# Kernel optimization log

Hardware: AMD Instinct MI355X
Metric: run time of the kernel (lower is better)

The kernel has to match this reference:

```python
import jax, jax.numpy as jnp
import numpy as np

N_CHANNELS = 8
SECTION = 32768
F_IN = 64
F_OUT = 64
UNITS = 512


def setup_inputs() -> dict:
    key = jax.random.key(0)
    ks = jax.random.split(key, 10)
    scale = lambda fan_in: 1.0 / np.sqrt(fan_in)
    return {
        "x": jax.random.normal(ks[0], (N_CHANNELS * SECTION, F_IN), jnp.float32),
        "w0": jax.random.normal(ks[1], (N_CHANNELS, UNITS, F_IN), jnp.float32) * scale(F_IN),
        "w1": jax.random.normal(ks[2], (N_CHANNELS, UNITS, UNITS), jnp.float32) * scale(UNITS),
        "w2": jax.random.normal(ks[3], (N_CHANNELS, UNITS, UNITS), jnp.float32) * scale(UNITS),
        "w3": jax.random.normal(ks[4], (N_CHANNELS, F_OUT, UNITS), jnp.float32) * scale(UNITS),
        "b0": jax.random.normal(ks[5], (N_CHANNELS, UNITS), jnp.float32) * 0.01,
        "b1": jax.random.normal(ks[6], (N_CHANNELS, UNITS), jnp.float32) * 0.01,
        "b2": jax.random.normal(ks[7], (N_CHANNELS, UNITS), jnp.float32) * 0.01,
        "b3": jax.random.normal(ks[8], (N_CHANNELS, F_OUT), jnp.float32) * 0.01,
        "section_size": SECTION,
    }


def reference(x, w0, w1, w2, w3, b0, b1, b2, b3, section_size):
    # Equal sections of size `section_size` per channel: reshape to [C, S, F]
    # and run the per-channel MLP as batched (grouped) GEMMs.
    C = w0.shape[0]
    xs = x.reshape(C, section_size, -1)  # [C, S, F_in]
    for w, b in ((w0, b0), (w1, b1), (w2, b2)):
        xs = jax.nn.relu(jnp.einsum('csi,coi->cso', xs, w) + b[:, None, :])
    ys = jnp.einsum('csi,coi->cso', xs, w3) + b3[:, None, :]  # [C, S, F_out]
    return ys.reshape(C * section_size, -1)
```

## Files before the change

### kernel.cpp

```cpp
#include <hip/hip_runtime.h>
#include <hip/hip_bf16.h>

#define CH 8
#define SEC 32768
#define FIN 64
#define FOUT 64
#define UN 512
#define BM 64

typedef __bf16 bf16;
typedef bf16 bf16x8 __attribute__((ext_vector_type(8)));
typedef bf16 bf16x4 __attribute__((ext_vector_type(4)));
typedef float f32x4 __attribute__((ext_vector_type(4)));

__device__ __forceinline__ bf16x8 cvt8(const float* __restrict__ src) {
  f32x4 u0 = *(const f32x4*)src;
  f32x4 u1 = *(const f32x4*)(src + 4);
  bf16x8 v;
  v[0] = (bf16)u0[0]; v[1] = (bf16)u0[1]; v[2] = (bf16)u0[2]; v[3] = (bf16)u0[3];
  v[4] = (bf16)u1[0]; v[5] = (bf16)u1[1]; v[6] = (bf16)u1[2]; v[7] = (bf16)u1[3];
  return v;
}

__device__ __forceinline__ void store_cvt8(void* dst, const float* __restrict__ src) {
  *(bf16x8*)dst = cvt8(src);
}

template<int K, bool WSPATH>
__device__ __forceinline__ void run_main_layer(
    const bf16* __restrict__ wb,
    const float* __restrict__ wf,
    const float* __restrict__ bias, char* __restrict__ act,
    int w, int l, int l15, int l4)
{
  constexpr int NKS = K / 32;
  const int col0 = w * 64;
  const char* abase = act + l * 16;

  f32x4 acc[4][4];
#pragma unroll
  for (int mt = 0; mt < 4; ++mt)
#pragma unroll
    for (int nt = 0; nt < 4; ++nt)
      acc[mt][nt] = f32x4{0.f, 0.f, 0.f, 0.f};

  if constexpr (WSPATH) {
    const bf16* bp = wb + ((size_t)(w * 4) * NKS * 64 + l) * 8;
    bf16x8 B0[4], B1[4];
#pragma unroll
    for (int i = 0; i < 4; ++i)
      B0[i] = *(const bf16x8*)(bp + (size_t)(i * NKS) * 512);

#pragma unroll
    for (int j = 0; j < NKS; j += 2) {
      if (j + 1 < NKS) {
#pragma unroll
        for (int i = 0; i < 4; ++i)
          B1[i] = *(const bf16x8*)(bp + (size_t)(i * NKS + j + 1) * 512);
      }
      {
        bf16x8 a[4];
#pragma unroll
        for (int mt = 0; mt < 4; ++mt)
          a[mt] = *(const bf16x8*)(abase + (mt * NKS + j) * 1024);
        __builtin_amdgcn_s_setprio(1);
#pragma unroll
        for (int mt = 0; mt < 4; ++mt)
#pragma unroll
          for (int nt = 0; nt < 4; ++nt)
            acc[mt][nt] = __builtin_amdgcn_mfma_f32_16x16x32_bf16(B0[nt], a[mt], acc[mt][nt], 0, 0, 0);
        __builtin_amdgcn_s_setprio(0);
      }
      if (j + 2 < NKS) {
#pragma unroll
        for (int i = 0; i < 4; ++i)
          B0[i] = *(const bf16x8*)(bp + (size_t)(i * NKS + j + 2) * 512);
      }
      if (j + 1 < NKS) {
        bf16x8 a[4];
#pragma unroll
        for (int mt = 0; mt < 4; ++mt)
          a[mt] = *(const bf16x8*)(abase + (mt * NKS + j + 1) * 1024);
        __builtin_amdgcn_s_setprio(1);
#pragma unroll
        for (int mt = 0; mt < 4; ++mt)
#pragma unroll
          for (int nt = 0; nt < 4; ++nt)
            acc[mt][nt] = __builtin_amdgcn_mfma_f32_16x16x32_bf16(B1[nt], a[mt], acc[mt][nt], 0, 0, 0);
        __builtin_amdgcn_s_setprio(0);
      }
    }
  } else {
    const float* bpf[4];
#pragma unroll
    for (int nt = 0; nt < 4; ++nt)
      bpf[nt] = wf + (size_t)(col0 + nt * 16 + l15) * K + l4 * 8;
#pragma unroll
    for (int j = 0; j < NKS; ++j) {
      bf16x8 a[4], b[4];
#pragma unroll
      for (int nt = 0; nt < 4; ++nt) b[nt] = cvt8(bpf[nt] + j * 32);
#pragma unroll
      for (int mt = 0; mt < 4; ++mt)
        a[mt] = *(const bf16x8*)(abase + (mt * NKS + j) * 1024);
#pragma unroll
      for (int mt = 0; mt < 4; ++mt)
#pragma unroll
        for (int nt = 0; nt < 4; ++nt)
          acc[mt][nt] = __builtin_amdgcn_mfma_f32_16x16x32_bf16(b[nt], a[mt], acc[mt][nt], 0, 0, 0);
    }
  }

  __syncthreads();

#pragma unroll
  for (int nt = 0; nt < 4; ++nt) {
    const f32x4 bv = *(const f32x4*)(bias + col0 + nt * 16 + l4 * 4);
    const int slot = l15 + ((nt & 1) * 2 + (l4 >> 1)) * 16;
    const int ksp  = w * 2 + (nt >> 1);
    const int boff = slot * 16 + (l4 & 1) * 8;
#pragma unroll
    for (int mt = 0; mt < 4; ++mt) {
      bf16x4 pk;
#pragma unroll
      for (int r = 0; r < 4; ++r) {
        const float v = acc[mt][nt][r] + bv[r];
        pk[r] = (bf16)(v > 0.f ? v : 0.f);
      }
      *(bf16x4*)(act + (mt * 16 + ksp) * 1024 + boff) = pk;
    }
  }
  __syncthreads();
}

template<bool WSPATH>
__device__ __forceinline__ void run_final_layer(
    const bf16* __restrict__ wb, const float* __restrict__ wf,
    const float* __restrict__ bias, const char* __restrict__ act,
    float* __restrict__ gout,
    int w, int l, int l15, int l4)
{
  constexpr int NKS = 16;
  const int mt = w >> 1;
  const int nb = (w & 1) * 2;
  const char* abase = act + mt * 16384 + l * 16;

  f32x4 acc[2];
  acc[0] = f32x4{0.f, 0.f, 0.f, 0.f};
  acc[1] = f32x4{0.f, 0.f, 0.f, 0.f};

  if constexpr (WSPATH) {
    const bf16* bp0 = wb + ((size_t)(nb + 0) * 16 * 64 + l) * 8;
    const bf16* bp1 = wb + ((size_t)(nb + 1) * 16 * 64 + l) * 8;
    bf16x8 B0[2], B1[2];
    B0[0] = *(const bf16x8*)(bp0);
    B0[1] = *(const bf16x8*)(bp1);
#pragma unroll
    for (int j = 0; j < NKS; j += 2) {
      {
        B1[0] = *(const bf16x8*)(bp0 + (size_t)(j + 1) * 512);
        B1[1] = *(const bf16x8*)(bp1 + (size_t)(j + 1) * 512);
        const bf16x8 a = *(const bf16x8*)(abase + j * 1024);
        acc[0] = __builtin_amdgcn_mfma_f32_16x16x32_bf16(B0[0], a, acc[0], 0, 0, 0);
        acc[1] = __builtin_amdgcn_mfma_f32_16x16x32_bf16(B0[1], a, acc[1], 0, 0, 0);
      }
      {
        if (j + 2 < NKS) {
          B0[0] = *(const bf16x8*)(bp0 + (size_t)(j + 2) * 512);
          B0[1] = *(const bf16x8*)(bp1 + (size_t)(j + 2) * 512);
        }
        const bf16x8 a = *(const bf16x8*)(abase + (j + 1) * 1024);
        acc[0] = __builtin_amdgcn_mfma_f32_16x16x32_bf16(B1[0], a, acc[0], 0, 0, 0);
        acc[1] = __builtin_amdgcn_mfma_f32_16x16x32_bf16(B1[1], a, acc[1], 0, 0, 0);
      }
    }
  } else {
    const float* bpf0 = wf + (size_t)((nb + 0) * 16 + l15) * UN + l4 * 8;
    const float* bpf1 = wf + (size_t)((nb + 1) * 16 + l15) * UN + l4 * 8;
#pragma unroll
    for (int j = 0; j < NKS; ++j) {
      const bf16x8 b0 = cvt8(bpf0 + j * 32);
      const bf16x8 b1 = cvt8(bpf1 + j * 32);
      const bf16x8 a = *(const bf16x8*)(abase + j * 1024);
      acc[0] = __builtin_amdgcn_mfma_f32_16x16x32_bf16(b0, a, acc[0], 0, 0, 0);
      acc[1] = __builtin_amdgcn_mfma_f32_16x16x32_bf16(b1, a, acc[1], 0, 0, 0);
    }
  }

#pragma unroll
  for (int i = 0; i < 2; ++i) {
    const f32x4 bv = *(const f32x4*)(bias + (nb + i) * 16 + l4 * 4);
    f32x4 o;
#pragma unroll
    for (int r = 0; r < 4; ++r) o[r] = acc[i][r] + bv[r];
    *(f32x4*)(gout + (size_t)(mt * 16 + l15) * FOUT + (nb + i) * 16 + l4 * 4) = o;
  }
}

template<bool WSPATH>
__global__ __launch_bounds__(512, 2) void mlp_fused(
    const float* __restrict__ x,
    const float* __restrict__ w0f, const float* __restrict__ w1f,
    const float* __restrict__ w2f, const float* __restrict__ w3f,
    const float* __restrict__ b0, const float* __restrict__ b1,
    const float* __restrict__ b2, const float* __restrict__ b3,
    const bf16* __restrict__ wbase,
    float* __restrict__ out)
{
  extern __shared__ char smem[];
  char* act = smem;

  const int tid = threadIdx.x;
  const int w = tid >> 6, l = tid & 63;
  const int l15 = l & 15, l4 = l >> 4;

  const int wg = (blockIdx.x & 7) * 512 + (blockIdx.x >> 3);
  const int ch = wg >> 9;
  const int row0 = (wg & 511) * BM;

  const bf16* w0b = wbase + (size_t)ch * UN * FIN;
  const bf16* w1b = wbase + CH * UN * FIN + (size_t)ch * UN * UN;
  const bf16* w2b = wbase + CH * UN * FIN + CH * UN * UN + (size_t)ch * UN * UN;
  const bf16* w3b = wbase + CH * UN * FIN + 2 * CH * UN * UN + (size_t)ch * FOUT * UN;
  const float* w0c = w0f + (size_t)ch * UN * FIN;
  const float* w1c = w1f + (size_t)ch * UN * UN;
  const float* w2c = w2f + (size_t)ch * UN * UN;
  const float* w3c = w3f + (size_t)ch * FOUT * UN;
  const float* b0c = b0 + ch * UN;
  const float* b1c = b1 + ch * UN;
  const float* b2c = b2 + ch * UN;
  const float* b3c = b3 + ch * FOUT;

  {
    const float* xs = x + (size_t)(ch * SEC + row0) * FIN;
    store_cvt8(act + w * 1024 + l * 16,
               xs + ((w >> 1) * 16 + l15) * FIN + (w & 1) * 32 + l4 * 8);
  }
  __syncthreads();

  run_main_layer<64,  WSPATH>(w0b, w0c, b0c, act, w, l, l15, l4);
  run_main_layer<512, WSPATH>(w1b, w1c, b1c, act, w, l, l15, l4);
  run_main_layer<512, WSPATH>(w2b, w2c, b2c, act, w, l, l15, l4);
  run_final_layer<WSPATH>(w3b, w3c, b3c, act,
                          out + (size_t)(ch * SEC + row0) * FOUT,
                          w, l, l15, l4);
}

template<int K, int N>
__device__ __forceinline__ void cvt_one(const float* __restrict__ src,
                                        bf16* __restrict__ dst, int t)
{
  constexpr int NKS = K / 32;
  constexpr int perCh = N * K / 8;
  const int ch = t / perCh;
  const int r = t - ch * perCh;
  const int l = r & 63;
  const int p = r >> 6;
  const int ks = p & (NKS - 1);
  const int f = p / NKS;
  const float* s = src + (size_t)ch * N * K + (size_t)(f * 16 + (l & 15)) * K
                 + ks * 32 + (l >> 4) * 8;
  store_cvt8(dst + (size_t)t * 8, s);
}

__global__ void cvt_weights(const float* __restrict__ w0, const float* __restrict__ w1,
                            const float* __restrict__ w2, const float* __restrict__ w3,
                            bf16* __restrict__ o)
{
  constexpr int T0 = CH * UN * FIN / 8;
  constexpr int T1 = CH * UN * UN / 8;
  constexpr int total = 2 * T0 + 2 * T1;
  for (int t = blockIdx.x * blockDim.x + threadIdx.x; t < total;
       t += gridDim.x * blockDim.x) {
    if (t < T0)                cvt_one<FIN, UN>(w0, o, t);
    else if (t < T0 + T1)      cvt_one<UN, UN>(w1, o + CH * UN * FIN, t - T0);
    else if (t < T0 + 2 * T1)  cvt_one<UN, UN>(w2, o + CH * UN * FIN + CH * UN * UN, t - T0 - T1);
    else                       cvt_one<UN, FOUT>(w3, o + CH * UN * FIN + 2 * CH * UN * UN, t - T0 - 2 * T1);
  }
}

extern "C" void kernel_launch(void* const* d_in, const int* in_sizes, int n_in,
                              void* d_out, int out_size, void* d_ws, size_t ws_size,
                              hipStream_t stream)
{
  const float* x  = (const float*)d_in[0];
  const float* w0 = (const float*)d_in[1];
  const float* w1 = (const float*)d_in[2];
  const float* w2 = (const float*)d_in[3];
  const float* w3 = (const float*)d_in[4];
  const float* b0 = (const float*)d_in[5];
  const float* b1 = (const float*)d_in[6];
  const float* b2 = (const float*)d_in[7];
  const float* b3 = (const float*)d_in[8];
  float* out = (float*)d_out;

  const int grid = CH * (SEC / BM);
  const size_t wbytes = (size_t)(2 * CH * UN * FIN + 2 * CH * UN * UN) * 2;

  if (ws_size >= wbytes) {
    bf16* wb = (bf16*)d_ws;
    hipLaunchKernelGGL(cvt_weights, dim3(2304), dim3(256), 0, stream, w0, w1, w2, w3, wb);
    hipFuncSetAttribute(reinterpret_cast<const void*>(mlp_fused<true>),
                        hipFuncAttributeMaxDynamicSharedMemorySize, 65536);
    hipLaunchKernelGGL(mlp_fused<true>, dim3(grid), dim3(512), 65536, stream,
                       x, w0, w1, w2, w3, b0, b1, b2, b3, wb, out);
  } else {
    hipFuncSetAttribute(reinterpret_cast<const void*>(mlp_fused<false>),
                        hipFuncAttributeMaxDynamicSharedMemorySize, 65536);
    hipLaunchKernelGGL(mlp_fused<false>, dim3(grid), dim3(512), 65536, stream,
                       x, w0, w1, w2, w3, b0, b1, b2, b3, (const bf16*)nullptr, out);
  }
}
```

Before: 302.8 us.

## Double row tile to 128 with 16-wave 2x8 warp grid per block

Raises the rows per block from 64 to 128 and launches 1024-thread blocks, with waves arranged as 2 row groups by 8 column groups. Each weight fragment loaded from global memory now feeds twice as many rows, which cuts weight traffic per row. The final layer is remapped so each wave handles one 16-column group across two row tiles. In exchange the block needs 128KB of LDS, the manual double-buffered weight prefetch is removed, and the launch bounds of (1024, 4) may force a very low register budget and cause spills.

```diff
diff --git a/kernel.cpp b/kernel.cpp
--- a/kernel.cpp
+++ b/kernel.cpp
@@ -6,7 +6,7 @@
 #define FIN 64
 #define FOUT 64
 #define UN 512
-#define BM 64
+#define BM 128
 
 typedef __bf16 bf16;
 typedef bf16 bf16x8 __attribute__((ext_vector_type(8)));
@@ -31,11 +31,11 @@
     const bf16* __restrict__ wb,
     const float* __restrict__ wf,
     const float* __restrict__ bias, char* __restrict__ act,
-    int w, int l, int l15, int l4)
+    int w, int l, int l15, int l4, int wm, int wn)
 {
   constexpr int NKS = K / 32;
-  const int col0 = w * 64;
-  const char* abase = act + l * 16;
+  const int col0 = wn * 64;
+  const char* abase = act + wm * (4 * NKS * 1024) + l * 16;
 
   f32x4 acc[4][4];
 #pragma unroll
@@ -45,50 +45,23 @@
       acc[mt][nt] = f32x4{0.f, 0.f, 0.f, 0.f};
 
   if constexpr (WSPATH) {
-    const bf16* bp = wb + ((size_t)(w * 4) * NKS * 64 + l) * 8;
-    bf16x8 B0[4], B1[4];
-#pragma unroll
-    for (int i = 0; i < 4; ++i)
-      B0[i] = *(const bf16x8*)(bp + (size_t)(i * NKS) * 512);
-
-#pragma unroll
-    for (int j = 0; j < NKS; j += 2) {
-      if (j + 1 < NKS) {
-#pragma unroll
-        for (int i = 0; i < 4; ++i)
-          B1[i] = *(const bf16x8*)(bp + (size_t)(i * NKS + j + 1) * 512);
-      }
-      {
-        bf16x8 a[4];
-#pragma unroll
-        for (int mt = 0; mt < 4; ++mt)
-          a[mt] = *(const bf16x8*)(abase + (mt * NKS + j) * 1024);
-        __builtin_amdgcn_s_setprio(1);
-#pragma unroll
-        for (int mt = 0; mt < 4; ++mt)
-#pragma unroll
-          for (int nt = 0; nt < 4; ++nt)
-            acc[mt][nt] = __builtin_amdgcn_mfma_f32_16x16x32_bf16(B0[nt], a[mt], acc[mt][nt], 0, 0, 0);
-        __builtin_amdgcn_s_setprio(0);
-      }
-      if (j + 2 < NKS) {
-#pragma unroll
-        for (int i = 0; i < 4; ++i)
-          B0[i] = *(const bf16x8*)(bp + (size_t)(i * NKS + j + 2) * 512);
-      }
-      if (j + 1 < NKS) {
-        bf16x8 a[4];
-#pragma unroll
-        for (int mt = 0; mt < 4; ++mt)
-          a[mt] = *(const bf16x8*)(abase + (mt * NKS + j + 1) * 1024);
-        __builtin_amdgcn_s_setprio(1);
-#pragma unroll
-        for (int mt = 0; mt < 4; ++mt)
-#pragma unroll
-          for (int nt = 0; nt < 4; ++nt)
-            acc[mt][nt] = __builtin_amdgcn_mfma_f32_16x16x32_bf16(B1[nt], a[mt], acc[mt][nt], 0, 0, 0);
-        __builtin_amdgcn_s_setprio(0);
-      }
+    const bf16* bp = wb + ((size_t)(wn * 4) * NKS * 64 + l) * 8;
+#pragma unroll
+    for (int j = 0; j < NKS; ++j) {
+      bf16x8 B[4], a[4];
+#pragma unroll
+      for (int i = 0; i < 4; ++i)
+        B[i] = *(const bf16x8*)(bp + (size_t)(i * NKS + j) * 512);
+#pragma unroll
+      for (int mt = 0; mt < 4; ++mt)
+        a[mt] = *(const bf16x8*)(abase + (mt * NKS + j) * 1024);
+      __builtin_amdgcn_s_setprio(1);
+#pragma unroll
+      for (int mt = 0; mt < 4; ++mt)
+#pragma unroll
+        for (int nt = 0; nt < 4; ++nt)
+          acc[mt][nt] = __builtin_amdgcn_mfma_f32_16x16x32_bf16(B[nt], a[mt], acc[mt][nt], 0, 0, 0);
+      __builtin_amdgcn_s_setprio(0);
     }
   } else {
     const float* bpf[4];
@@ -117,7 +90,7 @@
   for (int nt = 0; nt < 4; ++nt) {
     const f32x4 bv = *(const f32x4*)(bias + col0 + nt * 16 + l4 * 4);
     const int slot = l15 + ((nt & 1) * 2 + (l4 >> 1)) * 16;
-    const int ksp  = w * 2 + (nt >> 1);
+    const int ksp  = wn * 2 + (nt >> 1);
     const int boff = slot * 16 + (l4 & 1) * 8;
 #pragma unroll
     for (int mt = 0; mt < 4; ++mt) {
@@ -127,7 +100,7 @@
         const float v = acc[mt][nt][r] + bv[r];
         pk[r] = (bf16)(v > 0.f ? v : 0.f);
       }
-      *(bf16x4*)(act + (mt * 16 + ksp) * 1024 + boff) = pk;
+      *(bf16x4*)(act + ((wm * 4 + mt) * 16 + ksp) * 1024 + boff) = pk;
     }
   }
   __syncthreads();
@@ -141,64 +114,47 @@
     int w, int l, int l15, int l4)
 {
   constexpr int NKS = 16;
-  const int mt = w >> 1;
-  const int nb = (w & 1) * 2;
-  const char* abase = act + mt * 16384 + l * 16;
+  const int rg = w >> 2, cg = w & 3;
+  const char* abase = act + (rg * 2) * (NKS * 1024) + l * 16;
 
   f32x4 acc[2];
   acc[0] = f32x4{0.f, 0.f, 0.f, 0.f};
   acc[1] = f32x4{0.f, 0.f, 0.f, 0.f};
 
   if constexpr (WSPATH) {
-    const bf16* bp0 = wb + ((size_t)(nb + 0) * 16 * 64 + l) * 8;
-    const bf16* bp1 = wb + ((size_t)(nb + 1) * 16 * 64 + l) * 8;
-    bf16x8 B0[2], B1[2];
-    B0[0] = *(const bf16x8*)(bp0);
-    B0[1] = *(const bf16x8*)(bp1);
-#pragma unroll
-    for (int j = 0; j < NKS; j += 2) {
-      {
-        B1[0] = *(const bf16x8*)(bp0 + (size_t)(j + 1) * 512);
-        B1[1] = *(const bf16x8*)(bp1 + (size_t)(j + 1) * 512);
-        const bf16x8 a = *(const bf16x8*)(abase + j * 1024);
-        acc[0] = __builtin_amdgcn_mfma_f32_16x16x32_bf16(B0[0], a, acc[0], 0, 0, 0);
-        acc[1] = __builtin_amdgcn_mfma_f32_16x16x32_bf16(B0[1], a, acc[1], 0, 0, 0);
-      }
-      {
-        if (j + 2 < NKS) {
-          B0[0] = *(const bf16x8*)(bp0 + (size_t)(j + 2) * 512);
-          B0[1] = *(const bf16x8*)(bp1 + (size_t)(j + 2) * 512);
-        }
-        const bf16x8 a = *(const bf16x8*)(abase + (j + 1) * 1024);
-        acc[0] = __builtin_amdgcn_mfma_f32_16x16x32_bf16(B1[0], a, acc[0], 0, 0, 0);
-        acc[1] = __builtin_amdgcn_mfma_f32_16x16x32_bf16(B1[1], a, acc[1], 0, 0, 0);
-      }
+    const bf16* bp = wb + ((size_t)cg * 16 * 64 + l) * 8;
+#pragma unroll
+    for (int j = 0; j < NKS; ++j) {
+      const bf16x8 b  = *(const bf16x8*)(bp + (size_t)j * 512);
+      const bf16x8 a0 = *(const bf16x8*)(abase + j * 1024);
+      const bf16x8 a1 = *(const bf16x8*)(abase + (NKS + j) * 1024);
+      acc[0] = __builtin_amdgcn_mfma_f32_16x16x32_bf16(b, a0, acc[0], 0, 0, 0);
+      acc[1] = __builtin_amdgcn_mfma_f32_16x16x32_bf16(b, a1, acc[1], 0, 0, 0);
     }
   } else {
-    const float* bpf0 = wf + (size_t)((nb + 0) * 16 + l15) * UN + l4 * 8;
-    const float* bpf1 = wf + (size_t)((nb + 1) * 16 + l15) * UN + l4 * 8;
-#pragma unroll
-    for (int j = 0; j < NKS; ++j) {
-      const bf16x8 b0 = cvt8(bpf0 + j * 32);
-      const bf16x8 b1 = cvt8(bpf1 + j * 32);
-      const bf16x8 a = *(const bf16x8*)(abase + j * 1024);
-      acc[0] = __builtin_amdgcn_mfma_f32_16x16x32_bf16(b0, a, acc[0], 0, 0, 0);
-      acc[1] = __builtin_amdgcn_mfma_f32_16x16x32_bf16(b1, a, acc[1], 0, 0, 0);
-    }
-  }
-
+    const float* bpf = wf + (size_t)(cg * 16 + l15) * UN + l4 * 8;
+#pragma unroll
+    for (int j = 0; j < NKS; ++j) {
+      const bf16x8 b  = cvt8(bpf + j * 32);
+      const bf16x8 a0 = *(const bf16x8*)(abase + j * 1024);
+      const bf16x8 a1 = *(const bf16x8*)(abase + (NKS + j) * 1024);
+      acc[0] = __builtin_amdgcn_mfma_f32_16x16x32_bf16(b, a0, acc[0], 0, 0, 0);
+      acc[1] = __builtin_amdgcn_mfma_f32_16x16x32_bf16(b, a1, acc[1], 0, 0, 0);
+    }
+  }
+
+  const f32x4 bv = *(const f32x4*)(bias + cg * 16 + l4 * 4);
 #pragma unroll
   for (int i = 0; i < 2; ++i) {
-    const f32x4 bv = *(const f32x4*)(bias + (nb + i) * 16 + l4 * 4);
     f32x4 o;
 #pragma unroll
     for (int r = 0; r < 4; ++r) o[r] = acc[i][r] + bv[r];
-    *(f32x4*)(gout + (size_t)(mt * 16 + l15) * FOUT + (nb + i) * 16 + l4 * 4) = o;
+    *(f32x4*)(gout + (size_t)((rg * 2 + i) * 16 + l15) * FOUT + cg * 16 + l4 * 4) = o;
   }
 }
 
 template<bool WSPATH>
-__global__ __launch_bounds__(512, 2) void mlp_fused(
+__global__ __launch_bounds__(1024, 4) void mlp_fused(
     const float* __restrict__ x,
     const float* __restrict__ w0f, const float* __restrict__ w1f,
     const float* __restrict__ w2f, const float* __restrict__ w3f,
@@ -213,10 +169,11 @@
   const int tid = threadIdx.x;
   const int w = tid >> 6, l = tid & 63;
   const int l15 = l & 15, l4 = l >> 4;
-
-  const int wg = (blockIdx.x & 7) * 512 + (blockIdx.x >> 3);
-  const int ch = wg >> 9;
-  const int row0 = (wg & 511) * BM;
+  const int wm = w >> 3, wn = w & 7;
+
+  const int wg = (blockIdx.x & 7) * 256 + (blockIdx.x >> 3);
+  const int ch = wg >> 8;
+  const int row0 = (wg & 255) * BM;
 
   const bf16* w0b = wbase + (size_t)ch * UN * FIN;
   const bf16* w1b = wbase + CH * UN * FIN + (size_t)ch * UN * UN;
@@ -238,9 +195,9 @@
   }
   __syncthreads();
 
-  run_main_layer<64,  WSPATH>(w0b, w0c, b0c, act, w, l, l15, l4);
-  run_main_layer<512, WSPATH>(w1b, w1c, b1c, act, w, l, l15, l4);
-  run_main_layer<512, WSPATH>(w2b, w2c, b2c, act, w, l, l15, l4);
+  run_main_layer<64,  WSPATH>(w0b, w0c, b0c, act, w, l, l15, l4, wm, wn);
+  run_main_layer<512, WSPATH>(w1b, w1c, b1c, act, w, l, l15, l4, wm, wn);
+  run_main_layer<512, WSPATH>(w2b, w2c, b2c, act, w, l, l15, l4, wm, wn);
   run_final_layer<WSPATH>(w3b, w3c, b3c, act,
                           out + (size_t)(ch * SEC + row0) * FOUT,
                           w, l, l15, l4);
@@ -301,13 +258,13 @@
     bf16* wb = (bf16*)d_ws;
     hipLaunchKernelGGL(cvt_weights, dim3(2304), dim3(256), 0, stream, w0, w1, w2, w3, wb);
     hipFuncSetAttribute(reinterpret_cast<const void*>(mlp_fused<true>),
-                        hipFuncAttributeMaxDynamicSharedMemorySize, 65536);
-    hipLaunchKernelGGL(mlp_fused<true>, dim3(grid), dim3(512), 65536, stream,
+                        hipFuncAttributeMaxDynamicSharedMemorySize, 131072);
+    hipLaunchKernelGGL(mlp_fused<true>, dim3(grid), dim3(1024), 131072, stream,
                        x, w0, w1, w2, w3, b0, b1, b2, b3, wb, out);
   } else {
     hipFuncSetAttribute(reinterpret_cast<const void*>(mlp_fused<false>),
-                        hipFuncAttributeMaxDynamicSharedMemorySize, 65536);
-    hipLaunchKernelGGL(mlp_fused<false>, dim3(grid), dim3(512), 65536, stream,
+                        hipFuncAttributeMaxDynamicSharedMemorySize, 131072);
+    hipLaunchKernelGGL(mlp_fused<false>, dim3(grid), dim3(1024), 131072, stream,
                        x, w0, w1, w2, w3, b0, b1, b2, b3, (const bf16*)nullptr, out);
   }
 }
```

New measurement: 288.8 us. 1.05x faster.
